# Kernel tuning notes

Measured on AMD Instinct MI355X. Metric: run time of the kernel, lower is better.

The kernel has to match this reference:

```python
import jax, jax.numpy as jnp
import numpy as np

N_NODES = 50000
N_EDGES = 800000
IN_DIM = 128
HIDDEN = 128
NUM_CLASSES = 64
NEG_SLOPE = 0.2


def setup_inputs() -> dict:
    key = jax.random.key(0)
    ks = jax.random.split(key, 12)
    x = jax.random.normal(ks[0], (N_NODES, IN_DIM), dtype=jnp.float32)
    src = jax.random.randint(ks[1], (N_EDGES,), 0, N_NODES, dtype=jnp.int64)
    dst = jax.random.randint(ks[2], (N_EDGES,), 0, N_NODES, dtype=jnp.int64)
    def glorot(k, shape):
        fan_in, fan_out = shape[0], shape[-1]
        s = jnp.sqrt(2.0 / (fan_in + fan_out)).astype(jnp.float32)
        return jax.random.normal(k, shape, dtype=jnp.float32) * s
    return {
        "x": x, "src": src, "dst": dst,
        # GATConv params (1 head, no bias, no residual)
        "W_gat": glorot(ks[3], (IN_DIM, HIDDEN)),
        "attn_l": glorot(ks[4], (HIDDEN,)),
        "attn_r": glorot(ks[5], (HIDDEN,)),
        # GraphConv params (norm='none', bias=True)
        "W1": glorot(ks[6], (HIDDEN, HIDDEN)),
        "b1": jnp.zeros((HIDDEN,), dtype=jnp.float32),
        "W2": glorot(ks[7], (HIDDEN, HIDDEN)),
        "b2": jnp.zeros((HIDDEN,), dtype=jnp.float32),
        "Wc": glorot(ks[8], (HIDDEN, NUM_CLASSES)),
        "bc": jnp.zeros((NUM_CLASSES,), dtype=jnp.float32),
    }


def reference(x, src, dst, W_gat, attn_l, attn_r, W1, b1, W2, b2, Wc, bc):
    N = x.shape[0]
    # --- GATConv, single head, eval mode (dropout=0) ---
    h = x @ W_gat                      # (N, H)
    el = h @ attn_l                    # (N,)
    er = h @ attn_r                    # (N,)
    e = jax.nn.leaky_relu(el[src] + er[dst], negative_slope=NEG_SLOPE)  # (E,)
    # edge softmax over incoming edges of each dst node
    emax = jax.ops.segment_max(e, dst, num_segments=N)
    ee = jnp.exp(e - emax[dst])
    esum = jax.ops.segment_sum(ee, dst, num_segments=N)
    alpha = ee / esum[dst]             # (E,) attention = reused edge weights
    h1 = jax.ops.segment_sum(h[src] * alpha[:, None], dst, num_segments=N)
    h1 = jax.nn.elu(h1)                # GATConv activation

    # --- GraphConv (norm='none') with edge_weight = alpha ---
    def gconv(hin, W, b):
        hp = hin @ W                                   # project (order is math-equivalent)
        agg = jax.ops.segment_sum(hp[src] * alpha[:, None], dst, num_segments=N)
        return agg + b

    h2 = gconv(h1, W1, b1)
    h3 = gconv(h2, W2, b2)
    logits = gconv(h3, Wc, bc)         # (N, num_classes)
    return logits
```

## Files before the change

### kernel.cpp

```cpp
#include <hip/hip_runtime.h>
#include <hip/hip_fp16.h>
#include <math.h>

#define N_NODES 50000
#define N_EDGES 800000
#define PAD_EDGES (N_EDGES + 16 * N_NODES)

typedef _Float16 half8 __attribute__((ext_vector_type(8)));
typedef float floatx16 __attribute__((ext_vector_type(16)));

#define NPREPA_BLK 129
#define NPREPP_BLK 33
#define NEDGE_BLK 3125
#define NSCAN_BLK 196
#define NGEMM_BLK 391

__global__ __launch_bounds__(256) void k1_prep_hist(const int* __restrict__ dst,
                                                    const float* __restrict__ Wg,
                                                    const float* __restrict__ W1,
                                                    const float* __restrict__ W2,
                                                    const float* __restrict__ b1,
                                                    int* __restrict__ deg,
                                                    int* __restrict__ rank,
                                                    __half* __restrict__ Wg_hl,
                                                    float* __restrict__ W12,
                                                    float* __restrict__ c12) {
  int b = blockIdx.x;
  if (b >= NPREPA_BLK) {
    int e = (b - NPREPA_BLK) * 256 + threadIdx.x;
    if (e < N_EDGES) rank[e] = atomicAdd(&deg[dst[e]], 1);
    return;
  }
  int e = b * 256 + threadIdx.x;
  if (e < 16384) {
    _Float16* o = (_Float16*)Wg_hl;
    int k = e >> 7, n = e & 127;
    float w = Wg[k * 128 + n];
    _Float16 hi = (_Float16)w;
    float lo = w - (float)hi;
    int oi = (((k >> 3) * 128 + n) << 3) | (k & 7);
    o[oi] = hi;
    o[16384 + oi] = (_Float16)lo;
  } else if (e < 32768) {
    int local = e - 16384;
    int k = local >> 7, n = local & 127;
    float acc = 0.f;
    for (int j = 0; j < 128; ++j) acc = fmaf(W1[k * 128 + j], W2[j * 128 + n], acc);
    W12[k * 128 + n] = acc;
  } else if (e < 32896) {
    int n = e - 32768;
    float acc = 0.f;
    for (int j = 0; j < 128; ++j) acc = fmaf(b1[j], W2[j * 128 + n], acc);
    c12[n] = acc;
  }
}

__global__ __launch_bounds__(256) void scan1_k(const int* __restrict__ deg,
                                               int* __restrict__ offs,
                                               int* __restrict__ bsum,
                                               float2* __restrict__ el2, int N) {
  __shared__ int s[256];
  int t = threadIdx.x;
  int i = blockIdx.x * 256 + t;
  int v = 0;
  if (i < N) {
    int d = deg[i];
    v = (d + 15) & ~15;
    if (v < 16) v = 16;
    reinterpret_cast<float*>(el2)[2 * i + 1] = (d > 0) ? 1.f : 0.f;
  }
  s[t] = v;
  __syncthreads();
  for (int o = 1; o < 256; o <<= 1) {
    int add = (t >= o) ? s[t - o] : 0;
    __syncthreads();
    s[t] += add;
    __syncthreads();
  }
  if (i < N) offs[i] = s[t] - v;
  if (t == 255) bsum[blockIdx.x] = s[255];
}

__global__ __launch_bounds__(256) void scan3_k(int* __restrict__ offs,
                                               const int* __restrict__ deg,
                                               const int* __restrict__ bsum,
                                               int N, int nb) {
  __shared__ int s[256];
  int t = threadIdx.x;
  int b = blockIdx.x;
  s[t] = (t < nb && t < b) ? bsum[t] : 0;
  __syncthreads();
  for (int o = 128; o; o >>= 1) {
    if (t < o) s[t] += s[t + o];
    __syncthreads();
  }
  int base = s[0];
  int i = b * 256 + t;
  if (i < N) {
    int o = offs[i] + base;
    offs[i] = o;
    if (i == N - 1) {
      int d = deg[i];
      int pd = (d + 15) & ~15;
      if (pd < 16) pd = 16;
      offs[N] = o + pd;
    }
  }
}

template <int NCOL, bool A16, bool ELR>
__device__ __forceinline__ void mgemm_body(int bid, const void* __restrict__ Ap,
                                           const __half* __restrict__ Whl,
                                           __half* __restrict__ C16, int M,
                                           const float* __restrict__ al,
                                           const float* __restrict__ ar,
                                           float* __restrict__ el2x,
                                           float* __restrict__ er) {
  __shared__ __half Al[16][129][8];
  const int tid  = threadIdx.x;
  const int row0 = bid * 128;
  const int lane = tid & 63;
  const int lane31 = lane & 31;
  const int q = lane >> 5;
  const int r = tid >> 6;

  if (A16) {
    const uint4* A8 = (const uint4*)Ap;
    #pragma unroll
    for (int i = 0; i < 8; ++i) {
      int idx = tid + i * 256;
      int row = idx >> 4, c = idx & 15;
      int grow = row0 + row;
      uint4 v = make_uint4(0u, 0u, 0u, 0u);
      if (grow < M) v = A8[grow * 16 + c];
      *reinterpret_cast<uint4*>(&Al[c][row][0]) = v;
    }
  } else {
    const float4* A4 = (const float4*)Ap;
    #pragma unroll
    for (int i = 0; i < 8; ++i) {
      int idx = tid + i * 256;
      int row = idx >> 4, c = idx & 15;
      int grow = row0 + row;
      half8 hv = {};
      if (grow < M) {
        float4 a0 = A4[grow * 32 + c * 2];
        float4 a1 = A4[grow * 32 + c * 2 + 1];
        hv[0] = (_Float16)a0.x; hv[1] = (_Float16)a0.y;
        hv[2] = (_Float16)a0.z; hv[3] = (_Float16)a0.w;
        hv[4] = (_Float16)a1.x; hv[5] = (_Float16)a1.y;
        hv[6] = (_Float16)a1.z; hv[7] = (_Float16)a1.w;
      }
      *reinterpret_cast<half8*>(&Al[c][row][0]) = hv;
    }
  }
  __syncthreads();

  half8 afr[8];
  #pragma unroll
  for (int s = 0; s < 8; ++s)
    afr[s] = *reinterpret_cast<const half8*>(&Al[2 * s + q][r * 32 + lane31][0]);

  const half8* B8 = reinterpret_cast<const half8*>(Whl);
  const int KN8 = 16 * NCOL;

  float elp[16], erp[16];
  if (ELR) {
    #pragma unroll
    for (int i = 0; i < 16; ++i) { elp[i] = 0.f; erp[i] = 0.f; }
  }

  #pragma unroll
  for (int tc = 0; tc < NCOL / 32; ++tc) {
    floatx16 acc = {};
    int nbase = tc * 32 + lane31;
    #pragma unroll
    for (int s = 0; s < 8; ++s) {
      int ci = (2 * s + q) * NCOL + nbase;
      half8 bl = B8[KN8 + ci];
      half8 bh = B8[ci];
      acc = __builtin_amdgcn_mfma_f32_32x32x16_f16(afr[s], bl, acc, 0, 0, 0);
      acc = __builtin_amdgcn_mfma_f32_32x32x16_f16(afr[s], bh, acc, 0, 0, 0);
    }
    if (ELR) {
      float alv = al[nbase], arv = ar[nbase];
      #pragma unroll
      for (int i = 0; i < 16; ++i) {
        elp[i] = fmaf(acc[i], alv, elp[i]);
        erp[i] = fmaf(acc[i], arv, erp[i]);
      }
    }
    #pragma unroll
    for (int i = 0; i < 16; ++i) {
      int rl = (i & 3) + 8 * (i >> 2) + 4 * q;
      int grow = row0 + r * 32 + rl;
      if (grow < M) C16[grow * NCOL + nbase] = __float2half(acc[i]);
    }
  }

  if (ELR) {
    #pragma unroll
    for (int off = 1; off <= 16; off <<= 1) {
      #pragma unroll
      for (int i = 0; i < 16; ++i) {
        elp[i] += __shfl_xor(elp[i], off);
        erp[i] += __shfl_xor(erp[i], off);
      }
    }
    if (lane31 == 0) {
      #pragma unroll
      for (int i = 0; i < 16; ++i) {
        int rl = (i & 3) + 8 * (i >> 2) + 4 * q;
        int grow = row0 + r * 32 + rl;
        if (grow < M) {
          er[grow] = erp[i];
          el2x[2 * grow] = elp[i];
        }
      }
    }
  }
}

__global__ __launch_bounds__(256) void k4_fused(const int* __restrict__ src,
                                                const int* __restrict__ dst,
                                                const int* __restrict__ offs,
                                                const int* __restrict__ rank,
                                                int* __restrict__ csr_src,
                                                const float* __restrict__ W12,
                                                const float* __restrict__ c12,
                                                const float* __restrict__ Wc,
                                                const float* __restrict__ b2,
                                                __half* __restrict__ WPhl,
                                                float* __restrict__ c1,
                                                float* __restrict__ c2,
                                                const float* __restrict__ x,
                                                const __half* __restrict__ Wg_hl,
                                                __half* __restrict__ P16,
                                                const float* __restrict__ al,
                                                const float* __restrict__ ar,
                                                float2* __restrict__ el2,
                                                float* __restrict__ er, int N) {
  int b = blockIdx.x;
  if (b >= NPREPP_BLK + NGEMM_BLK) {
    int e = (b - NPREPP_BLK - NGEMM_BLK) * 256 + threadIdx.x;
    if (e < N_EDGES) {
      csr_src[offs[dst[e]] + rank[e]] = src[e];
    }
    return;
  }
  if (b >= NPREPP_BLK) {
    mgemm_body<128, false, true>(b - NPREPP_BLK, x, Wg_hl, P16, N, al, ar,
                                 reinterpret_cast<float*>(el2), er);
    return;
  }
  int e = b * 256 + threadIdx.x;
  _Float16* o = (_Float16*)WPhl;
  if (e < 8192) {
    int k = e >> 6, n = e & 63;
    float acc = 0.f;
    for (int j = 0; j < 128; ++j) acc = fmaf(W12[k * 128 + j], Wc[j * 64 + n], acc);
    _Float16 hi = (_Float16)acc;
    float lo = acc - (float)hi;
    int oi = (((k >> 3) * 64 + n) << 3) | (k & 7);
    o[oi] = hi;
    o[8192 + oi] = (_Float16)lo;
  } else if (e < 8256) {
    int n = e - 8192;
    float acc = 0.f;
    for (int j = 0; j < 128; ++j) acc = fmaf(c12[j], Wc[j * 64 + n], acc);
    c1[n] = acc;
  } else if (e < 8320) {
    int n = e - 8256;
    float acc = 0.f;
    for (int j = 0; j < 128; ++j) acc = fmaf(b2[j], Wc[j * 64 + n], acc);
    c2[n] = acc;
  }
}

__global__ __launch_bounds__(256) void mgemm64_k(const void* __restrict__ Ap,
                                                 const __half* __restrict__ Whl,
                                                 __half* __restrict__ C16, int M) {
  mgemm_body<64, true, false>(blockIdx.x, Ap, Whl, C16, M, nullptr, nullptr, nullptr, nullptr);
}

__device__ inline void fma8(float2 acc[4], uint4 u, float a) {
  __half2* h = reinterpret_cast<__half2*>(&u);
  #pragma unroll
  for (int j = 0; j < 4; ++j) {
    float2 f = __half22float2(h[j]);
    acc[j].x = fmaf(a, f.x, acc[j].x);
    acc[j].y = fmaf(a, f.y, acc[j].y);
  }
}

__global__ __launch_bounds__(256) void aggsm_k(const int* __restrict__ offs,
                                               const int* __restrict__ deg,
                                               const int* __restrict__ csr_src,
                                               const float2* __restrict__ el2,
                                               const float* __restrict__ er,
                                               int2* __restrict__ meta,
                                               float* __restrict__ t,
                                               const __half* __restrict__ hp,
                                               __half* __restrict__ out, int N) {
  __shared__ int2 lmeta[4][64];
  int wv   = threadIdx.x >> 6;
  int w    = (blockIdx.x * 256 + threadIdx.x) >> 6;
  int lane = threadIdx.x & 63;
  if (w >= N) return;
  int o0   = offs[w];
  int pcnt = offs[w + 1] - o0;
  int cnt  = deg[w];
  int q  = lane >> 4;
  int fl = lane & 15;
  const uint4* hpq = reinterpret_cast<const uint4*>(hp);

  if (cnt <= 64) {
    bool valid = lane < cnt;
    float erv = er[w];
    int s = 0;
    float ev = -3.4e38f, flag = 0.f;
    if (valid) {
      s = csr_src[o0 + lane];
      float2 e2 = el2[s];
      float e0 = e2.x + erv;
      ev = (e0 >= 0.f) ? e0 : 0.2f * e0;
      flag = e2.y;
    }
    float m = ev;
    #pragma unroll
    for (int off = 32; off; off >>= 1) m = fmaxf(m, __shfl_xor(m, off));
    float ee = valid ? __expf(ev - m) : 0.f;
    float sum = ee, tp = ee * flag;
    #pragma unroll
    for (int off = 32; off; off >>= 1) {
      sum += __shfl_xor(sum, off);
      tp  += __shfl_xor(tp, off);
    }
    float inv = (cnt > 0) ? 1.f / sum : 0.f;
    int2 mm = make_int2(0, 0);
    if (valid) mm = make_int2(s * 16, __float_as_int(ee * inv));
    if (lane < pcnt) meta[o0 + lane] = mm;
    lmeta[wv][lane] = mm;
    if (lane == 0) t[w] = tp * inv;
  } else {
    float erv = er[w];
    float m = -3.4e38f;
    for (int i = lane; i < cnt; i += 64) {
      int s = csr_src[o0 + i];
      float2 e2 = el2[s];
      float ev = e2.x + erv;
      ev = (ev >= 0.f) ? ev : 0.2f * ev;
      m = fmaxf(m, ev);
    }
    #pragma unroll
    for (int off = 32; off; off >>= 1) m = fmaxf(m, __shfl_xor(m, off));
    float sum = 0.f, tacc = 0.f;
    int myS = 0; float myE = 0.f;
    for (int i = lane; i < cnt; i += 64) {
      int s = csr_src[o0 + i];
      float2 e2 = el2[s];
      float ev = e2.x + erv;
      ev = (ev >= 0.f) ? ev : 0.2f * ev;
      float ee = __expf(ev - m);
      meta[o0 + i] = make_int2(s * 16, __float_as_int(ee));
      sum += ee;
      tacc += ee * e2.y;
      if (i == lane) { myS = s; myE = ee; }
    }
    #pragma unroll
    for (int off = 32; off; off >>= 1) {
      sum  += __shfl_xor(sum, off);
      tacc += __shfl_xor(tacc, off);
    }
    float inv = 1.f / sum;
    if (lane == 0) t[w] = tacc * inv;
    for (int i = lane; i < cnt; i += 64) {
      int2 mm = meta[o0 + i];
      meta[o0 + i] = make_int2(mm.x, __float_as_int(__int_as_float(mm.y) * inv));
    }
    for (int i = cnt + lane; i < pcnt; i += 64) meta[o0 + i] = make_int2(0, 0);
    lmeta[wv][lane] = make_int2(myS * 16, __float_as_int(myE * inv));
  }

  float2 acc0[4] = {}, acc1[4] = {};
  int pc = pcnt < 64 ? pcnt : 64;
  int2 mA = lmeta[wv][q], mB = lmeta[wv][4 + q];
  for (int base = 8; base < pc; base += 8) {
    int2 nA = lmeta[wv][base + q], nB = lmeta[wv][base + 4 + q];
    uint4 vA = hpq[mA.x + fl], vB = hpq[mB.x + fl];
    fma8(acc0, vA, __int_as_float(mA.y));
    fma8(acc1, vB, __int_as_float(mB.y));
    mA = nA; mB = nB;
  }
  {
    uint4 vA = hpq[mA.x + fl], vB = hpq[mB.x + fl];
    fma8(acc0, vA, __int_as_float(mA.y));
    fma8(acc1, vB, __int_as_float(mB.y));
  }
  for (int p = o0 + 64 + q; p < o0 + pcnt; p += 4) {
    int2 mm = meta[p];
    fma8(acc0, hpq[mm.x + fl], __int_as_float(mm.y));
  }
  #pragma unroll
  for (int j = 0; j < 4; ++j) { acc0[j].x += acc1[j].x; acc0[j].y += acc1[j].y; }
  #pragma unroll
  for (int off = 16; off <= 32; off <<= 1) {
    #pragma unroll
    for (int j = 0; j < 4; ++j) {
      acc0[j].x += __shfl_xor(acc0[j].x, off);
      acc0[j].y += __shfl_xor(acc0[j].y, off);
    }
  }
  if (q == 0) {
    float o8[8];
    #pragma unroll
    for (int j = 0; j < 4; ++j) { o8[2 * j] = acc0[j].x; o8[2 * j + 1] = acc0[j].y; }
    #pragma unroll
    for (int j = 0; j < 8; ++j) o8[j] = (o8[j] > 0.f) ? o8[j] : (__expf(o8[j]) - 1.f);
    __half2 p0 = __floats2half2_rn(o8[0], o8[1]);
    __half2 p1 = __floats2half2_rn(o8[2], o8[3]);
    __half2 p2 = __floats2half2_rn(o8[4], o8[5]);
    __half2 p3 = __floats2half2_rn(o8[6], o8[7]);
    uint4 pk;
    pk.x = *reinterpret_cast<unsigned*>(&p0);
    pk.y = *reinterpret_cast<unsigned*>(&p1);
    pk.z = *reinterpret_cast<unsigned*>(&p2);
    pk.w = *reinterpret_cast<unsigned*>(&p3);
    *reinterpret_cast<uint4*>(&out[w * 128 + fl * 8]) = pk;
  }
}

template <bool FINAL>
__global__ __launch_bounds__(256) void agg64v_k(const int* __restrict__ offs,
                                                const int2* __restrict__ meta,
                                                const __half* __restrict__ zp,
                                                const float* __restrict__ t,
                                                const int* __restrict__ deg,
                                                const float* __restrict__ c1,
                                                const float* __restrict__ c2,
                                                const float* __restrict__ bc,
                                                void* __restrict__ outp, int N) {
  int w    = (blockIdx.x * 256 + threadIdx.x) >> 6;
  int lane = threadIdx.x & 63;
  if (w >= N) return;
  int o0 = offs[w], o1 = offs[w + 1];
  int o   = lane >> 3;
  int fl  = lane & 7;
  const uint4* hpq = reinterpret_cast<const uint4*>(zp);

  float2 acc0[4] = {}, acc1[4] = {};
  int p = o0 + o;
  int2 mA = meta[p], mB = meta[p + 8];
  for (; p + 16 < o1; p += 16) {
    int2 nA = meta[p + 16], nB = meta[p + 24];
    uint4 vA = hpq[(mA.x >> 1) + fl];
    uint4 vB = hpq[(mB.x >> 1) + fl];
    fma8(acc0, vA, __int_as_float(mA.y));
    fma8(acc1, vB, __int_as_float(mB.y));
    mA = nA; mB = nB;
  }
  {
    uint4 vA = hpq[(mA.x >> 1) + fl];
    uint4 vB = hpq[(mB.x >> 1) + fl];
    fma8(acc0, vA, __int_as_float(mA.y));
    fma8(acc1, vB, __int_as_float(mB.y));
  }
  #pragma unroll
  for (int j = 0; j < 4; ++j) { acc0[j].x += acc1[j].x; acc0[j].y += acc1[j].y; }
  #pragma unroll
  for (int off = 8; off <= 32; off <<= 1) {
    #pragma unroll
    for (int j = 0; j < 4; ++j) {
      acc0[j].x += __shfl_xor(acc0[j].x, off);
      acc0[j].y += __shfl_xor(acc0[j].y, off);
    }
  }
  if (o == 0) {
    float o8[8];
    #pragma unroll
    for (int j = 0; j < 4; ++j) { o8[2 * j] = acc0[j].x; o8[2 * j + 1] = acc0[j].y; }
    if (FINAL) {
      float tw = t[w];
      float dw = (deg[w] > 0) ? 1.f : 0.f;
      float4 a0 = reinterpret_cast<const float4*>(c1)[fl * 2];
      float4 a1 = reinterpret_cast<const float4*>(c1)[fl * 2 + 1];
      float4 d0 = reinterpret_cast<const float4*>(c2)[fl * 2];
      float4 d1 = reinterpret_cast<const float4*>(c2)[fl * 2 + 1];
      float4 b0 = reinterpret_cast<const float4*>(bc)[fl * 2];
      float4 b1v = reinterpret_cast<const float4*>(bc)[fl * 2 + 1];
      o8[0] += tw * a0.x + dw * d0.x + b0.x;
      o8[1] += tw * a0.y + dw * d0.y + b0.y;
      o8[2] += tw * a0.z + dw * d0.z + b0.z;
      o8[3] += tw * a0.w + dw * d0.w + b0.w;
      o8[4] += tw * a1.x + dw * d1.x + b1v.x;
      o8[5] += tw * a1.y + dw * d1.y + b1v.y;
      o8[6] += tw * a1.z + dw * d1.z + b1v.z;
      o8[7] += tw * a1.w + dw * d1.w + b1v.w;
      float4* of = reinterpret_cast<float4*>(outp);
      of[w * 16 + fl * 2]     = make_float4(o8[0], o8[1], o8[2], o8[3]);
      of[w * 16 + fl * 2 + 1] = make_float4(o8[4], o8[5], o8[6], o8[7]);
    } else {
      __half2 p0 = __floats2half2_rn(o8[0], o8[1]);
      __half2 p1 = __floats2half2_rn(o8[2], o8[3]);
      __half2 p2 = __floats2half2_rn(o8[4], o8[5]);
      __half2 p3 = __floats2half2_rn(o8[6], o8[7]);
      uint4 pk;
      pk.x = *reinterpret_cast<unsigned*>(&p0);
      pk.y = *reinterpret_cast<unsigned*>(&p1);
      pk.z = *reinterpret_cast<unsigned*>(&p2);
      pk.w = *reinterpret_cast<unsigned*>(&p3);
      reinterpret_cast<uint4*>(outp)[w * 8 + fl] = pk;
    }
  }
}

extern "C" void kernel_launch(void* const* d_in, const int* in_sizes, int n_in,
                              void* d_out, int out_size, void* d_ws, size_t ws_size,
                              hipStream_t stream) {
  const float* x      = (const float*)d_in[0];
  const int*   src    = (const int*)d_in[1];
  const int*   dst    = (const int*)d_in[2];
  const float* W_gat  = (const float*)d_in[3];
  const float* attn_l = (const float*)d_in[4];
  const float* attn_r = (const float*)d_in[5];
  const float* W1     = (const float*)d_in[6];
  const float* b1     = (const float*)d_in[7];
  const float* W2     = (const float*)d_in[8];
  const float* b2     = (const float*)d_in[9];
  const float* Wc     = (const float*)d_in[10];
  const float* bc     = (const float*)d_in[11];
  float* out = (float*)d_out;

  char* ws = (char*)d_ws;
  size_t off = 0;
  auto walloc = [&](size_t bytes) -> void* {
    void* p = ws + off;
    off += (bytes + 255) & ~size_t(255);
    return p;
  };
  __half* P16     = (__half*)walloc((size_t)N_NODES * 128 * 2);
  __half* F16     = (__half*)walloc((size_t)N_NODES * 128 * 2);
  float*  er      = (float*)walloc((size_t)N_NODES * 4);
  float2* el2     = (float2*)walloc((size_t)N_NODES * 8);
  float*  tbuf    = (float*)walloc((size_t)N_NODES * 4);
  int*    deg     = (int*)walloc((size_t)N_NODES * 4);
  int*    offs    = (int*)walloc((size_t)(N_NODES + 1) * 4);
  int*    rank    = (int*)walloc((size_t)N_EDGES * 4);
  int*    csr_src = (int*)walloc((size_t)PAD_EDGES * 4);
  int2*   meta    = (int2*)walloc((size_t)PAD_EDGES * 8);
  int*    bsum    = (int*)walloc(1024);
  __half* Wg_hl   = (__half*)walloc((size_t)32768 * 2);
  __half* WP_hl   = (__half*)walloc((size_t)16384 * 2);
  float*  W12     = (float*)walloc((size_t)16384 * 4);
  float*  c12     = (float*)walloc((size_t)128 * 4);
  float*  c1      = (float*)walloc((size_t)64 * 4);
  float*  c2      = (float*)walloc((size_t)64 * 4);

  hipMemsetAsync(deg, 0, (size_t)N_NODES * 4, stream);

  const dim3 blk(256);
  const int nwave_blocks = (N_NODES + 3) / 4;

  k1_prep_hist<<<dim3(NPREPA_BLK + NEDGE_BLK), blk, 0, stream>>>(
      dst, W_gat, W1, W2, b1, deg, rank, Wg_hl, W12, c12);
  scan1_k<<<dim3(NSCAN_BLK), blk, 0, stream>>>(deg, offs, bsum, el2, N_NODES);
  scan3_k<<<dim3(NSCAN_BLK), blk, 0, stream>>>(offs, deg, bsum, N_NODES, NSCAN_BLK);
  k4_fused<<<dim3(NPREPP_BLK + NGEMM_BLK + NEDGE_BLK), blk, 0, stream>>>(
      src, dst, offs, rank, csr_src, W12, c12, Wc, b2, WP_hl, c1, c2,
      x, Wg_hl, P16, attn_l, attn_r, el2, er, N_NODES);

  aggsm_k<<<dim3(nwave_blocks), blk, 0, stream>>>(offs, deg, csr_src, el2, er, meta, tbuf, P16, F16, N_NODES);
  mgemm64_k<<<dim3(NGEMM_BLK), blk, 0, stream>>>(F16, WP_hl, P16, N_NODES);
  agg64v_k<false><<<dim3(nwave_blocks), blk, 0, stream>>>(offs, meta, P16, nullptr, nullptr, nullptr, nullptr, nullptr, F16, N_NODES);
  agg64v_k<false><<<dim3(nwave_blocks), blk, 0, stream>>>(offs, meta, F16, nullptr, nullptr, nullptr, nullptr, nullptr, P16, N_NODES);
  agg64v_k<true><<<dim3(nwave_blocks), blk, 0, stream>>>(offs, meta, P16, tbuf, deg, c1, c2, bc, out, N_NODES);
}
```

Before: 263.3 us.

## Replace prefix-scan CSR build with fixed-capacity per-node buckets and overflow list

Drops the degree histogram, two scan kernels and the rank array. Each edge is placed directly into a fixed 64-slot bucket per destination node, using an atomic counter in the same pass that scatters it, and rare overflow edges go to a global list. This removes two kernel launches, a memset and one full pass over the edges. In exchange the meta buffer grows to N*64 entries with sparse strided access, high-degree nodes must scan the whole overflow list, and the CSR buffer now aliases F16, so correctness relies on F16 not being written until the aggregation kernel runs.

```diff
diff --git a/kernel.cpp b/kernel.cpp
--- a/kernel.cpp
+++ b/kernel.cpp
@@ -4,31 +4,34 @@
 
 #define N_NODES 50000
 #define N_EDGES 800000
-#define PAD_EDGES (N_EDGES + 16 * N_NODES)
+#define CAP 64
+#define OVF_CAP 65536
 
 typedef _Float16 half8 __attribute__((ext_vector_type(8)));
 typedef float floatx16 __attribute__((ext_vector_type(16)));
 
 #define NPREPA_BLK 129
+#define NZERO_BLK 587
 #define NPREPP_BLK 33
+#define NGEMM_BLK 391
 #define NEDGE_BLK 3125
-#define NSCAN_BLK 196
-#define NGEMM_BLK 391
-
-__global__ __launch_bounds__(256) void k1_prep_hist(const int* __restrict__ dst,
-                                                    const float* __restrict__ Wg,
+
+__global__ __launch_bounds__(256) void k0_prep_zero(const float* __restrict__ Wg,
                                                     const float* __restrict__ W1,
                                                     const float* __restrict__ W2,
                                                     const float* __restrict__ b1,
-                                                    int* __restrict__ deg,
-                                                    int* __restrict__ rank,
                                                     __half* __restrict__ Wg_hl,
                                                     float* __restrict__ W12,
-                                                    float* __restrict__ c12) {
+                                                    float* __restrict__ c12,
+                                                    int* __restrict__ deg,
+                                                    float* __restrict__ el2f,
+                                                    int* __restrict__ ovfn) {
   int b = blockIdx.x;
   if (b >= NPREPA_BLK) {
-    int e = (b - NPREPA_BLK) * 256 + threadIdx.x;
-    if (e < N_EDGES) rank[e] = atomicAdd(&deg[dst[e]], 1);
+    int i = (b - NPREPA_BLK) * 256 + threadIdx.x;
+    if (i < N_NODES) deg[i] = 0;
+    else if (i < 3 * N_NODES) el2f[i - N_NODES] = 0.f;
+    else if (i == 3 * N_NODES) *ovfn = 0;
     return;
   }
   int e = b * 256 + threadIdx.x;
@@ -55,59 +58,6 @@
   }
 }
 
-__global__ __launch_bounds__(256) void scan1_k(const int* __restrict__ deg,
-                                               int* __restrict__ offs,
-                                               int* __restrict__ bsum,
-                                               float2* __restrict__ el2, int N) {
-  __shared__ int s[256];
-  int t = threadIdx.x;
-  int i = blockIdx.x * 256 + t;
-  int v = 0;
-  if (i < N) {
-    int d = deg[i];
-    v = (d + 15) & ~15;
-    if (v < 16) v = 16;
-    reinterpret_cast<float*>(el2)[2 * i + 1] = (d > 0) ? 1.f : 0.f;
-  }
-  s[t] = v;
-  __syncthreads();
-  for (int o = 1; o < 256; o <<= 1) {
-    int add = (t >= o) ? s[t - o] : 0;
-    __syncthreads();
-    s[t] += add;
-    __syncthreads();
-  }
-  if (i < N) offs[i] = s[t] - v;
-  if (t == 255) bsum[blockIdx.x] = s[255];
-}
-
-__global__ __launch_bounds__(256) void scan3_k(int* __restrict__ offs,
-                                               const int* __restrict__ deg,
-                                               const int* __restrict__ bsum,
-                                               int N, int nb) {
-  __shared__ int s[256];
-  int t = threadIdx.x;
-  int b = blockIdx.x;
-  s[t] = (t < nb && t < b) ? bsum[t] : 0;
-  __syncthreads();
-  for (int o = 128; o; o >>= 1) {
-    if (t < o) s[t] += s[t + o];
-    __syncthreads();
-  }
-  int base = s[0];
-  int i = b * 256 + t;
-  if (i < N) {
-    int o = offs[i] + base;
-    offs[i] = o;
-    if (i == N - 1) {
-      int d = deg[i];
-      int pd = (d + 15) & ~15;
-      if (pd < 16) pd = 16;
-      offs[N] = o + pd;
-    }
-  }
-}
-
 template <int NCOL, bool A16, bool ELR>
 __device__ __forceinline__ void mgemm_body(int bid, const void* __restrict__ Ap,
                                            const __half* __restrict__ Whl,
@@ -221,11 +171,13 @@
   }
 }
 
-__global__ __launch_bounds__(256) void k4_fused(const int* __restrict__ src,
+__global__ __launch_bounds__(256) void k1_fused(const int* __restrict__ src,
                                                 const int* __restrict__ dst,
-                                                const int* __restrict__ offs,
-                                                const int* __restrict__ rank,
-                                                int* __restrict__ csr_src,
+                                                int* __restrict__ deg,
+                                                int* __restrict__ csr,
+                                                float* __restrict__ el2f,
+                                                int2* __restrict__ ovf,
+                                                int* __restrict__ ovfn,
                                                 const float* __restrict__ W12,
                                                 const float* __restrict__ c12,
                                                 const float* __restrict__ Wc,
@@ -244,7 +196,16 @@
   if (b >= NPREPP_BLK + NGEMM_BLK) {
     int e = (b - NPREPP_BLK - NGEMM_BLK) * 256 + threadIdx.x;
     if (e < N_EDGES) {
-      csr_src[offs[dst[e]] + rank[e]] = src[e];
+      int d = dst[e];
+      int s = src[e];
+      int r = atomicAdd(&deg[d], 1);
+      if (r == 0) el2f[2 * d + 1] = 1.0f;
+      if (r < CAP) {
+        csr[d * CAP + r] = s;
+      } else {
+        int j = atomicAdd(ovfn, 1);
+        if (j < OVF_CAP) ovf[j] = make_int2(d, s);
+      }
     }
     return;
   }
@@ -293,12 +254,14 @@
   }
 }
 
-__global__ __launch_bounds__(256) void aggsm_k(const int* __restrict__ offs,
-                                               const int* __restrict__ deg,
-                                               const int* __restrict__ csr_src,
+__global__ __launch_bounds__(256) void aggsm_k(const int* __restrict__ deg,
+                                               const int* __restrict__ csr,
                                                const float2* __restrict__ el2,
                                                const float* __restrict__ er,
                                                int2* __restrict__ meta,
+                                               int2* __restrict__ meta_ovf,
+                                               const int2* __restrict__ ovf,
+                                               const int* __restrict__ ovfn,
                                                float* __restrict__ t,
                                                const __half* __restrict__ hp,
                                                __half* __restrict__ out, int N) {
@@ -307,20 +270,22 @@
   int w    = (blockIdx.x * 256 + threadIdx.x) >> 6;
   int lane = threadIdx.x & 63;
   if (w >= N) return;
-  int o0   = offs[w];
-  int pcnt = offs[w + 1] - o0;
-  int cnt  = deg[w];
+  int o0  = w * CAP;
+  int cnt = deg[w];
   int q  = lane >> 4;
   int fl = lane & 15;
   const uint4* hpq = reinterpret_cast<const uint4*>(hp);
 
-  if (cnt <= 64) {
+  int pcnt;
+  if (cnt <= CAP) {
+    pcnt = (cnt + 15) & ~15;
+    if (pcnt < 16) pcnt = 16;
     bool valid = lane < cnt;
     float erv = er[w];
     int s = 0;
     float ev = -3.4e38f, flag = 0.f;
     if (valid) {
-      s = csr_src[o0 + lane];
+      s = csr[o0 + lane];
       float2 e2 = el2[s];
       float e0 = e2.x + erv;
       ev = (e0 >= 0.f) ? e0 : 0.2f * e0;
@@ -343,29 +308,39 @@
     lmeta[wv][lane] = mm;
     if (lane == 0) t[w] = tp * inv;
   } else {
+    pcnt = CAP;
+    int ovn = *ovfn;
+    if (ovn > OVF_CAP) ovn = OVF_CAP;
     float erv = er[w];
-    float m = -3.4e38f;
-    for (int i = lane; i < cnt; i += 64) {
-      int s = csr_src[o0 + i];
-      float2 e2 = el2[s];
-      float ev = e2.x + erv;
-      ev = (ev >= 0.f) ? ev : 0.2f * ev;
-      m = fmaxf(m, ev);
+    int s0 = csr[o0 + lane];
+    float2 e20 = el2[s0];
+    float ev0 = e20.x + erv;
+    ev0 = (ev0 >= 0.f) ? ev0 : 0.2f * ev0;
+    float m = ev0;
+    for (int j = lane; j < ovn; j += 64) {
+      int2 ov = ovf[j];
+      if (ov.x == w) {
+        float2 e2 = el2[ov.y];
+        float ev = e2.x + erv;
+        ev = (ev >= 0.f) ? ev : 0.2f * ev;
+        m = fmaxf(m, ev);
+      }
     }
     #pragma unroll
     for (int off = 32; off; off >>= 1) m = fmaxf(m, __shfl_xor(m, off));
-    float sum = 0.f, tacc = 0.f;
-    int myS = 0; float myE = 0.f;
-    for (int i = lane; i < cnt; i += 64) {
-      int s = csr_src[o0 + i];
-      float2 e2 = el2[s];
-      float ev = e2.x + erv;
-      ev = (ev >= 0.f) ? ev : 0.2f * ev;
-      float ee = __expf(ev - m);
-      meta[o0 + i] = make_int2(s * 16, __float_as_int(ee));
-      sum += ee;
-      tacc += ee * e2.y;
-      if (i == lane) { myS = s; myE = ee; }
+    float ee0 = __expf(ev0 - m);
+    float sum = ee0, tacc = ee0 * e20.y;
+    for (int j = lane; j < ovn; j += 64) {
+      int2 ov = ovf[j];
+      if (ov.x == w) {
+        float2 e2 = el2[ov.y];
+        float ev = e2.x + erv;
+        ev = (ev >= 0.f) ? ev : 0.2f * ev;
+        float ee = __expf(ev - m);
+        meta_ovf[j] = make_int2(ov.y * 16, __float_as_int(ee));
+        sum += ee;
+        tacc += ee * e2.y;
+      }
     }
     #pragma unroll
     for (int off = 32; off; off >>= 1) {
@@ -374,16 +349,19 @@
     }
     float inv = 1.f / sum;
     if (lane == 0) t[w] = tacc * inv;
-    for (int i = lane; i < cnt; i += 64) {
-      int2 mm = meta[o0 + i];
-      meta[o0 + i] = make_int2(mm.x, __float_as_int(__int_as_float(mm.y) * inv));
-    }
-    for (int i = cnt + lane; i < pcnt; i += 64) meta[o0 + i] = make_int2(0, 0);
-    lmeta[wv][lane] = make_int2(myS * 16, __float_as_int(myE * inv));
+    int2 mm = make_int2(s0 * 16, __float_as_int(ee0 * inv));
+    meta[o0 + lane] = mm;
+    lmeta[wv][lane] = mm;
+    for (int j = lane; j < ovn; j += 64) {
+      if (ovf[j].x == w) {
+        int2 t2 = meta_ovf[j];
+        meta_ovf[j] = make_int2(t2.x, __float_as_int(__int_as_float(t2.y) * inv));
+      }
+    }
   }
 
   float2 acc0[4] = {}, acc1[4] = {};
-  int pc = pcnt < 64 ? pcnt : 64;
+  int pc = pcnt;
   int2 mA = lmeta[wv][q], mB = lmeta[wv][4 + q];
   for (int base = 8; base < pc; base += 8) {
     int2 nA = lmeta[wv][base + q], nB = lmeta[wv][base + 4 + q];
@@ -397,9 +375,15 @@
     fma8(acc0, vA, __int_as_float(mA.y));
     fma8(acc1, vB, __int_as_float(mB.y));
   }
-  for (int p = o0 + 64 + q; p < o0 + pcnt; p += 4) {
-    int2 mm = meta[p];
-    fma8(acc0, hpq[mm.x + fl], __int_as_float(mm.y));
+  if (cnt > CAP) {
+    int ovn = *ovfn;
+    if (ovn > OVF_CAP) ovn = OVF_CAP;
+    for (int j = q; j < ovn; j += 4) {
+      if (ovf[j].x == w) {
+        int2 mm2 = meta_ovf[j];
+        fma8(acc0, hpq[mm2.x + fl], __int_as_float(mm2.y));
+      }
+    }
   }
   #pragma unroll
   for (int j = 0; j < 4; ++j) { acc0[j].x += acc1[j].x; acc0[j].y += acc1[j].y; }
@@ -431,11 +415,13 @@
 }
 
 template <bool FINAL>
-__global__ __launch_bounds__(256) void agg64v_k(const int* __restrict__ offs,
+__global__ __launch_bounds__(256) void agg64v_k(const int* __restrict__ deg,
                                                 const int2* __restrict__ meta,
+                                                const int2* __restrict__ meta_ovf,
+                                                const int2* __restrict__ ovf,
+                                                const int* __restrict__ ovfn,
                                                 const __half* __restrict__ zp,
                                                 const float* __restrict__ t,
-                                                const int* __restrict__ deg,
                                                 const float* __restrict__ c1,
                                                 const float* __restrict__ c2,
                                                 const float* __restrict__ bc,
@@ -443,7 +429,11 @@
   int w    = (blockIdx.x * 256 + threadIdx.x) >> 6;
   int lane = threadIdx.x & 63;
   if (w >= N) return;
-  int o0 = offs[w], o1 = offs[w + 1];
+  int dv = deg[w];
+  int pc = (dv + 15) & ~15;
+  if (pc < 16) pc = 16;
+  if (pc > CAP) pc = CAP;
+  int o0 = w * CAP, o1 = w * CAP + pc;
   int o   = lane >> 3;
   int fl  = lane & 7;
   const uint4* hpq = reinterpret_cast<const uint4*>(zp);
@@ -465,6 +455,16 @@
     fma8(acc0, vA, __int_as_float(mA.y));
     fma8(acc1, vB, __int_as_float(mB.y));
   }
+  if (dv > CAP) {
+    int ovn = *ovfn;
+    if (ovn > OVF_CAP) ovn = OVF_CAP;
+    for (int j = o; j < ovn; j += 8) {
+      if (ovf[j].x == w) {
+        int2 mm2 = meta_ovf[j];
+        fma8(acc0, hpq[(mm2.x >> 1) + fl], __int_as_float(mm2.y));
+      }
+    }
+  }
   #pragma unroll
   for (int j = 0; j < 4; ++j) { acc0[j].x += acc1[j].x; acc0[j].y += acc1[j].y; }
   #pragma unroll
@@ -481,7 +481,7 @@
     for (int j = 0; j < 4; ++j) { o8[2 * j] = acc0[j].x; o8[2 * j + 1] = acc0[j].y; }
     if (FINAL) {
       float tw = t[w];
-      float dw = (deg[w] > 0) ? 1.f : 0.f;
+      float dw = (dv > 0) ? 1.f : 0.f;
       float4 a0 = reinterpret_cast<const float4*>(c1)[fl * 2];
       float4 a1 = reinterpret_cast<const float4*>(c1)[fl * 2 + 1];
       float4 d0 = reinterpret_cast<const float4*>(c2)[fl * 2];
@@ -540,15 +540,15 @@
   };
   __half* P16     = (__half*)walloc((size_t)N_NODES * 128 * 2);
   __half* F16     = (__half*)walloc((size_t)N_NODES * 128 * 2);
+  int*    csr     = (int*)F16;
   float*  er      = (float*)walloc((size_t)N_NODES * 4);
   float2* el2     = (float2*)walloc((size_t)N_NODES * 8);
   float*  tbuf    = (float*)walloc((size_t)N_NODES * 4);
   int*    deg     = (int*)walloc((size_t)N_NODES * 4);
-  int*    offs    = (int*)walloc((size_t)(N_NODES + 1) * 4);
-  int*    rank    = (int*)walloc((size_t)N_EDGES * 4);
-  int*    csr_src = (int*)walloc((size_t)PAD_EDGES * 4);
-  int2*   meta    = (int2*)walloc((size_t)PAD_EDGES * 8);
-  int*    bsum    = (int*)walloc(1024);
+  int2*   meta    = (int2*)walloc((size_t)N_NODES * CAP * 8);
+  int2*   ovf     = (int2*)walloc((size_t)OVF_CAP * 8);
+  int2*   movf    = (int2*)walloc((size_t)OVF_CAP * 8);
+  int*    ovfn    = (int*)walloc(256);
   __half* Wg_hl   = (__half*)walloc((size_t)32768 * 2);
   __half* WP_hl   = (__half*)walloc((size_t)16384 * 2);
   float*  W12     = (float*)walloc((size_t)16384 * 4);
@@ -556,22 +556,20 @@
   float*  c1      = (float*)walloc((size_t)64 * 4);
   float*  c2      = (float*)walloc((size_t)64 * 4);
 
-  hipMemsetAsync(deg, 0, (size_t)N_NODES * 4, stream);
-
   const dim3 blk(256);
   const int nwave_blocks = (N_NODES + 3) / 4;
 
-  k1_prep_hist<<<dim3(NPREPA_BLK + NEDGE_BLK), blk, 0, stream>>>(
-      dst, W_gat, W1, W2, b1, deg, rank, Wg_hl, W12, c12);
-  scan1_k<<<dim3(NSCAN_BLK), blk, 0, stream>>>(deg, offs, bsum, el2, N_NODES);
-  scan3_k<<<dim3(NSCAN_BLK), blk, 0, stream>>>(offs, deg, bsum, N_NODES, NSCAN_BLK);
-  k4_fused<<<dim3(NPREPP_BLK + NGEMM_BLK + NEDGE_BLK), blk, 0, stream>>>(
-      src, dst, offs, rank, csr_src, W12, c12, Wc, b2, WP_hl, c1, c2,
+  k0_prep_zero<<<dim3(NPREPA_BLK + NZERO_BLK), blk, 0, stream>>>(
+      W_gat, W1, W2, b1, Wg_hl, W12, c12, deg, reinterpret_cast<float*>(el2), ovfn);
+  k1_fused<<<dim3(NPREPP_BLK + NGEMM_BLK + NEDGE_BLK), blk, 0, stream>>>(
+      src, dst, deg, csr, reinterpret_cast<float*>(el2), ovf, ovfn,
+      W12, c12, Wc, b2, WP_hl, c1, c2,
       x, Wg_hl, P16, attn_l, attn_r, el2, er, N_NODES);
 
-  aggsm_k<<<dim3(nwave_blocks), blk, 0, stream>>>(offs, deg, csr_src, el2, er, meta, tbuf, P16, F16, N_NODES);
+  aggsm_k<<<dim3(nwave_blocks), blk, 0, stream>>>(
+      deg, csr, el2, er, meta, movf, ovf, ovfn, tbuf, P16, F16, N_NODES);
   mgemm64_k<<<dim3(NGEMM_BLK), blk, 0, stream>>>(F16, WP_hl, P16, N_NODES);
-  agg64v_k<false><<<dim3(nwave_blocks), blk, 0, stream>>>(offs, meta, P16, nullptr, nullptr, nullptr, nullptr, nullptr, F16, N_NODES);
-  agg64v_k<false><<<dim3(nwave_blocks), blk, 0, stream>>>(offs, meta, F16, nullptr, nullptr, nullptr, nullptr, nullptr, P16, N_NODES);
-  agg64v_k<true><<<dim3(nwave_blocks), blk, 0, stream>>>(offs, meta, P16, tbuf, deg, c1, c2, bc, out, N_NODES);
-}
+  agg64v_k<false><<<dim3(nwave_blocks), blk, 0, stream>>>(deg, meta, movf, ovf, ovfn, P16, nullptr, nullptr, nullptr, nullptr, F16, N_NODES);
+  agg64v_k<false><<<dim3(nwave_blocks), blk, 0, stream>>>(deg, meta, movf, ovf, ovfn, F16, nullptr, nullptr, nullptr, nullptr, P16, N_NODES);
+  agg64v_k<true><<<dim3(nwave_blocks), blk, 0, stream>>>(deg, meta, movf, ovf, ovfn, P16, tbuf, c1, c2, bc, out, N_NODES);
+}
```

Measured after the change: 253.6 us. 3.7% less time.
